# Kernel tuning notes

Hardware: AMD Instinct MI355X
Metric: run time of the kernel (lower is better)

## Reference

```python
import jax, jax.numpy as jnp
import numpy as np

B, C, H, W = 4, 12, 256, 256
ALPHA = 2.0
LARGE = 1e6  # > any image dimension; sentinel for 'no feature pixel found yet'


def _dist_1d(feature):
    # feature: [..., L] bool. 1D distance along last axis to nearest True element.
    f = jnp.moveaxis(feature, -1, 0)  # [L, ...]
    init = jnp.full(f.shape[1:], LARGE, jnp.float32)

    def step(c, fi):
        c = jnp.where(fi, 0.0, jnp.minimum(c + 1.0, LARGE))
        return c, c

    _, fwd = jax.lax.scan(step, init, f)
    _, bwd = jax.lax.scan(step, init, f[::-1])
    fwd = jnp.moveaxis(fwd, 0, -1)
    bwd = jnp.moveaxis(bwd[::-1], 0, -1)
    return jnp.minimum(fwd, bwd)


def edt(mask):
    # Exact Euclidean distance transform, matching scipy distance_transform_edt:
    # mask: [N, H, W] bool; returns distance from each pixel to nearest False pixel
    # (0 at False pixels). Separable squared-EDT: 1D pass along rows, then an
    # exact min over column offsets: D2[i,j] = min_j' g2[i,j'] + (j-j')**2.
    feature = ~mask
    g = _dist_1d(jnp.swapaxes(feature, -1, -2))  # distance along H within each column
    g = jnp.swapaxes(g, -1, -2)                  # [N, H, W]
    g2 = g * g
    Wd = mask.shape[-1]
    jidx = jnp.arange(Wd, dtype=jnp.float32)     # [W]
    cols = jnp.moveaxis(g2, -1, 0)               # [W, N, H]

    def step(running, xs):
        col, t = xs                              # col: [N, H], t: scalar
        cand = col[..., None] + (jidx - t) ** 2  # [N, H, W]
        return jnp.minimum(running, cand), None

    init = jnp.full(g2.shape, LARGE * LARGE, jnp.float32)
    d2, _ = jax.lax.scan(step, init, (cols, jidx))
    return jnp.sqrt(d2)


def distance_field(mask):
    # mask: [N, H, W] bool. field = edt(fg) + edt(bg); zero if no fg pixel (as in torch).
    field = edt(mask) + edt(~mask)
    has_fg = jnp.any(mask, axis=(-2, -1))
    return jnp.where(has_fg[..., None, None], field, 0.0)


def setup_inputs() -> dict:
    key = jax.random.key(0)
    k1, k2 = jax.random.split(key)
    pred = jax.random.normal(k1, (B, C, H, W), dtype=jnp.float32)
    target = jax.random.randint(k2, (B, H, W), 0, C, dtype=jnp.int64)
    return {"pred": pred, "target": target}


def reference(pred, target):
    pred_all = jax.nn.softmax(pred, axis=1)                              # [B,C,H,W]
    target_all = jax.nn.one_hot(target, C, dtype=pred.dtype, axis=1)     # [B,C,H,W]
    # Distance fields are computed under torch.no_grad() -> constants here.
    masks = jnp.stack([pred_all > 0.5, target_all > 0.5], 0).reshape(-1, H, W)
    fields = jax.lax.stop_gradient(distance_field(masks))
    fields = fields.reshape(2, pred.shape[0], C, H, W)
    pred_dt, target_dt = fields[0], fields[1]
    distance = pred_dt ** ALPHA + target_dt ** ALPHA
    pred_error = (pred_all - target_all) ** 2
    # per-class mean over (B,H,W), summed over classes (matches the torch loop)
    loss_sum = jnp.sum(jnp.mean(pred_error * distance, axis=(0, 2, 3)))
    logp = jax.nn.log_softmax(pred, axis=1)
    ce = -jnp.mean(jnp.take_along_axis(logp, target[:, None], axis=1))
    return loss_sum / C / pred.shape[0] / 3.0 + ce
```

## Files before the change

### kernel.cpp

```cpp
#include <hip/hip_runtime.h>
#include <math.h>

constexpr int Bn = 4, Cn = 12, Hn = 256, Wn = 256;
constexpr int HWn  = Hn * Wn;
constexpr int NPIX = Bn * HWn;
constexpr int NPLANE = Bn * Cn;
constexpr int NMASK = 2 * NPLANE;
constexpr int NJOB  = 2 * NMASK;
constexpr float LARGEf = 1.0e6f;


__global__ void masks_kernel(const float* __restrict__ pred,
                             const int* __restrict__ target,
                             unsigned int* __restrict__ maskw,
                             float* __restrict__ err,
                             unsigned int* __restrict__ blockOr,
                             double* __restrict__ cepart) {
    int pix = blockIdx.x * blockDim.x + threadIdx.x;
    int b = pix >> 16;
    int p = pix & (HWn - 1);
    float v[Cn];
    float mx = -3.4e38f;
#pragma unroll
    for (int c = 0; c < Cn; ++c) {
        v[c] = pred[(size_t)(b * Cn + c) * HWn + p];
        mx = fmaxf(mx, v[c]);
    }
    int t = target[pix];
    float raw_t = 0.f, s = 0.f;
#pragma unroll
    for (int c = 0; c < Cn; ++c) {
        if (c == t) raw_t = v[c];
        v[c] = expf(v[c] - mx);
        s += v[c];
    }
    unsigned word = 1u << (Cn + t);
#pragma unroll
    for (int c = 0; c < Cn; ++c) {
        float prob = v[c] / s;
        int pb = (prob > 0.5f) ? 1 : 0;
        word |= (unsigned)pb << c;
        float oh = (c == t) ? 1.0f : 0.0f;
        float d = prob - oh;
        err[(size_t)(b * Cn + c) * HWn + p] = d * d;
    }
    maskw[pix] = word;
    float logp_t = raw_t - mx - logf(s);

    unsigned worw = word;
    for (int o = 32; o > 0; o >>= 1) worw |= __shfl_down(worw, o, 64);
    double ced = (double)logp_t;
    for (int o = 32; o > 0; o >>= 1) ced += __shfl_down(ced, o, 64);
    int lane = threadIdx.x & 63, wv = threadIdx.x >> 6;
    if (lane == 0) {
        blockOr[blockIdx.x * 4 + wv] = worw;
        cepart[blockIdx.x * 4 + wv] = ced;
    }
}

__device__ __forceinline__ int mask_has_fg(const unsigned int* fgflags, int m) {
    int mm = (m < NPLANE) ? m : m - NPLANE;
    int b = mm / Cn, c = mm % Cn;
    unsigned fg = (m < NPLANE) ? fgflags[b] : fgflags[4 + b];
    return (fg >> c) & 1;
}

constexpr int SEG  = 4;
constexpr int SEGR = Hn / SEG;
constexpr int STRb = 68;

__global__ void colpass_kernel(const unsigned int* __restrict__ maskw,
                               const unsigned int* __restrict__ blockOr,
                               unsigned char* __restrict__ gcol,
                               unsigned int* __restrict__ colmask,
                               unsigned int* __restrict__ fgflags) {
    int blk = blockIdx.x;
    int tid = threadIdx.x;
    int lane = tid & 63, wv = tid >> 6;
    if (blk == NMASK * 4) {
        unsigned acc = 0;
#pragma unroll
        for (int k = 0; k < 16; ++k) acc |= blockOr[wv * 1024 + k * 64 + lane];
        for (int o = 32; o > 0; o >>= 1) acc |= __shfl_down(acc, o, 64);
        if (lane == 0) {
            fgflags[wv] = acc & 0xFFFu;
            fgflags[4 + wv] = acc >> Cn;
        }
        return;
    }
    int m  = blk >> 2;
    int cg = blk & 3;
    int mm = (m < NPLANE) ? m : m - NPLANE;
    int b = mm / Cn, c = mm % Cn;
    unsigned bit = (m < NPLANE) ? (unsigned)c : (unsigned)(Cn + c);
    int s  = wv;
    int jl = lane;
    int j  = cg * 64 + jl;
    int r0 = s * SEGR;
    const unsigned int* mp = maskw + (size_t)b * HWn;
    unsigned char* gpA = gcol + (size_t)m * HWn;
    unsigned char* gpB = gcol + (size_t)(m + NMASK) * HWn;

    __shared__ unsigned char ldsFA[256 * STRb];
    __shared__ unsigned char ldsFB[256 * STRb];
    __shared__ float eFA[256], eFB[256], eBA[256], eBB[256];
    __shared__ unsigned char segEmptyA[256], segEmptyB[256];

    unsigned long long vbits = 0ull;
    float cdA = LARGEf, cdB = LARGEf;
    for (int i = 0; i < SEGR; ++i) {
        unsigned w = mp[(r0 + i) * Wn + j];
        unsigned f = (w >> bit) & 1u;
        vbits |= (unsigned long long)f << i;
        cdA = (!f) ? 0.f : fminf(cdA + 1.f, LARGEf);
        cdB = f ? 0.f : fminf(cdB + 1.f, LARGEf);
        ldsFA[tid * STRb + i] = (unsigned char)fminf(cdA, 255.f);
        ldsFB[tid * STRb + i] = (unsigned char)fminf(cdB, 255.f);
    }
    unsigned long long aBits = ~vbits;
    eFA[tid] = cdA;
    eFB[tid] = cdB;
    eBA[tid] = aBits ? (float)__builtin_ctzll(aBits) : LARGEf;
    eBB[tid] = vbits ? (float)__builtin_ctzll(vbits) : LARGEf;
    segEmptyA[tid] = (aBits == 0ull) ? 1 : 0;
    segEmptyB[tid] = (vbits == 0ull) ? 1 : 0;
    __syncthreads();
    if (s == 0) {
        int emA = segEmptyA[jl] & segEmptyA[64 + jl] & segEmptyA[128 + jl] & segEmptyA[192 + jl];
        int emB = segEmptyB[jl] & segEmptyB[64 + jl] & segEmptyB[128 + jl] & segEmptyB[192 + jl];
        unsigned long long ba = __ballot(emA);
        unsigned long long bb = __ballot(emB);
        if (jl == 0) {
            colmask[m * 8 + cg * 2]                 = (unsigned)ba;
            colmask[m * 8 + cg * 2 + 1]             = (unsigned)(ba >> 32);
            colmask[(m + NMASK) * 8 + cg * 2]       = (unsigned)bb;
            colmask[(m + NMASK) * 8 + cg * 2 + 1]   = (unsigned)(bb >> 32);
        }
    }
    float xA = LARGEf, xB = LARGEf;
    for (int sp = 0; sp < s; ++sp) {
        xA = fminf(eFA[sp * 64 + jl], fminf(xA + (float)SEGR, LARGEf));
        xB = fminf(eFB[sp * 64 + jl], fminf(xB + (float)SEGR, LARGEf));
    }
    float yA = LARGEf, yB = LARGEf;
    for (int sp = SEG - 1; sp > s; --sp) {
        yA = fminf(eBA[sp * 64 + jl], fminf(yA + (float)SEGR, LARGEf));
        yB = fminf(eBB[sp * 64 + jl], fminf(yB + (float)SEGR, LARGEf));
    }
    float cA = LARGEf, cB = LARGEf;
    for (int i = SEGR - 1; i >= 0; --i) {
        unsigned f = (unsigned)((vbits >> i) & 1ull);
        cA = (!f) ? 0.f : fminf(cA + 1.f, LARGEf);
        cB = f ? 0.f : fminf(cB + 1.f, LARGEf);
        unsigned char ufA = ldsFA[tid * STRb + i];
        unsigned char ufB = ldsFB[tid * STRb + i];
        float lfA = (ufA == 255u) ? LARGEf : (float)ufA;
        float lfB = (ufB == 255u) ? LARGEf : (float)ufB;
        float fA = fminf(lfA, fminf(xA + (float)(i + 1), LARGEf));
        float wA = fminf(cA,  fminf(yA + (float)(SEGR - i), LARGEf));
        float gA = fminf(fA, wA);
        float fB = fminf(lfB, fminf(xB + (float)(i + 1), LARGEf));
        float wB = fminf(cB,  fminf(yB + (float)(SEGR - i), LARGEf));
        float gB = fminf(fB, wB);
        gpA[(r0 + i) * Wn + j] = (unsigned char)fminf(gA, 255.f);
        gpB[(r0 + i) * Wn + j] = (unsigned char)fminf(gB, 255.f);
    }
}

constexpr int RPAD = 256;
constexpr int NROWBLK = NMASK * Hn;
constexpr int RPB = 4;

__device__ __forceinline__ void scan4(const float* __restrict__ base, float m[4]) {
    float k2 = 1.f;
    for (int k = 1; k < Wn; k += 2) {
        float mx = fmaxf(fmaxf(m[0], m[1]), fmaxf(m[2], m[3]));
        if (k2 >= mx) break;
        float k2b = k2 + (float)(2 * k + 1);
#pragma unroll
        for (int g = 0; g < 4; ++g) {
            const float* p = base + 64 * g;
            m[g] = fminf(m[g], k2  + p[-k]);
            m[g] = fminf(m[g], k2b + p[-k - 1]);
            m[g] = fminf(m[g], k2  + p[k]);
            m[g] = fminf(m[g], k2b + p[k + 1]);
        }
        k2 = k2b + (float)(2 * k + 3);
    }
}

__global__ void rowpass_kernel(const unsigned char* __restrict__ gcol,
                               const unsigned int* __restrict__ colmask,
                               const float* __restrict__ err,
                               const unsigned int* __restrict__ fgflags,
                               double* __restrict__ partials) {
    int blk = blockIdx.x;
    int tid = threadIdx.x;
    int lane = tid & 63, w = tid >> 6;
    int m = (blk * RPB) >> 8;
    if (!mask_has_fg(fgflags, m)) {
        if (tid < RPB) partials[blk * RPB + tid] = 0.0;
        return;
    }
    int job = blk * RPB + w;
    int i = job & (Hn - 1);
    const float X = 1e12f;
    __shared__ float lds[RPB][2][Wn + 2 * RPAD];
    float* rA = lds[w][0];
    float* rB = lds[w][1];

    int ep = (m < NPLANE) ? m : m - NPLANE;
    const float* epr = err + (size_t)ep * HWn + i * Wn;
    float e0 = epr[lane], e1 = epr[lane + 64];
    float e2 = epr[lane + 128], e3 = epr[lane + 192];

    const unsigned char* rp = gcol + (size_t)m * HWn + i * Wn;
    const unsigned char* rq = gcol + (size_t)(m + NMASK) * HWn + i * Wn;
    unsigned ua4 = ((const unsigned*)rp)[lane];
    unsigned ub4 = ((const unsigned*)rq)[lane];
    unsigned nibA = (colmask[m * 8 + (lane >> 3)] >> ((lane & 7) * 4)) & 0xFu;
    unsigned nibB = (colmask[(m + NMASK) * 8 + (lane >> 3)] >> ((lane & 7) * 4)) & 0xFu;
    float4 fa, fb;
    {
        unsigned g0 = ua4 & 0xFFu, g1 = (ua4 >> 8) & 0xFFu;
        unsigned g2 = (ua4 >> 16) & 0xFFu, g3 = ua4 >> 24;
        fa.x = (nibA & 1u) ? X : (float)(g0 * g0);
        fa.y = (nibA & 2u) ? X : (float)(g1 * g1);
        fa.z = (nibA & 4u) ? X : (float)(g2 * g2);
        fa.w = (nibA & 8u) ? X : (float)(g3 * g3);
        g0 = ub4 & 0xFFu; g1 = (ub4 >> 8) & 0xFFu;
        g2 = (ub4 >> 16) & 0xFFu; g3 = ub4 >> 24;
        fb.x = (nibB & 1u) ? X : (float)(g0 * g0);
        fb.y = (nibB & 2u) ? X : (float)(g1 * g1);
        fb.z = (nibB & 4u) ? X : (float)(g2 * g2);
        fb.w = (nibB & 8u) ? X : (float)(g3 * g3);
    }
    float4 xv = make_float4(X, X, X, X);
    ((float4*)rA)[lane] = xv;
    ((float4*)(rA + RPAD))[lane] = fa;
    ((float4*)(rA + RPAD + Wn))[lane] = xv;
    ((float4*)rB)[lane] = xv;
    ((float4*)(rB + RPAD))[lane] = fb;
    ((float4*)(rB + RPAD + Wn))[lane] = xv;
    __syncthreads();

    float mA[4], mB[4];
#pragma unroll
    for (int g = 0; g < 4; ++g) {
        mA[g] = rA[RPAD + lane + 64 * g];
        mB[g] = rB[RPAD + lane + 64 * g];
    }
    scan4(rA + RPAD + lane, mA);
    scan4(rB + RPAD + lane, mB);

    float ev[4] = {e0, e1, e2, e3};
    double v = 0.0;
#pragma unroll
    for (int g = 0; g < 4; ++g) {
        float f = sqrtf(mA[g]) + sqrtf(mB[g]);
        v += (double)(ev[g] * (f * f));
    }
    for (int o = 32; o > 0; o >>= 1) v += __shfl_down(v, o, 64);
    if (lane == 0) partials[job] = v;
}

__global__ void final_kernel(const double* __restrict__ partials,
                             const double* __restrict__ cepart,
                             float* __restrict__ out) {
    int tid = threadIdx.x;
    double a = 0.0, ce = 0.0;
    for (int idx = tid; idx < NROWBLK; idx += 1024) a += partials[idx];
    for (int idx = tid; idx < 4096; idx += 1024) ce += cepart[idx];
    __shared__ double sa[1024], sc[1024];
    sa[tid] = a; sc[tid] = ce;
    __syncthreads();
    for (int s = 512; s > 0; s >>= 1) {
        if (tid < s) { sa[tid] += sa[tid + s]; sc[tid] += sc[tid + s]; }
        __syncthreads();
    }
    if (tid == 0) {
        double loss_sum = sa[0] / (double)NPIX;
        double cem = -sc[0] / (double)NPIX;
        double res = loss_sum / (double)Cn / (double)Bn / 3.0 + cem;
        out[0] = (float)res;
    }
}

extern "C" void kernel_launch(void* const* d_in, const int* in_sizes, int n_in,
                              void* d_out, int out_size, void* d_ws, size_t ws_size,
                              hipStream_t stream) {
    const float* pred  = (const float*)d_in[0];
    const int* target  = (const int*)d_in[1];
    float* out = (float*)d_out;
    char* ws = (char*)d_ws;

    unsigned int* maskw = (unsigned int*)ws;
    size_t off = (size_t)NPIX * 4;
    float* err = (float*)(ws + off);
    off += (size_t)NPLANE * HWn * 4;
    unsigned char* gcol = (unsigned char*)(ws + off);
    off += (size_t)NJOB * HWn;
    unsigned int* colmask = (unsigned int*)(ws + off);
    off += (size_t)NJOB * 8 * 4;
    unsigned int* fgflags = (unsigned int*)(ws + off);
    off += 512;
    unsigned int* blockOr = (unsigned int*)(ws + off);
    off += 4096 * 4;
    double* partials = (double*)(ws + off);
    off += (size_t)NROWBLK * 8;
    double* cepart = (double*)(ws + off);

    masks_kernel<<<NPIX / 256, 256, 0, stream>>>(pred, target, maskw, err,
                                                 blockOr, cepart);
    colpass_kernel<<<NMASK * 4 + 1, 256, 0, stream>>>(maskw, blockOr, gcol,
                                                      colmask, fgflags);
    rowpass_kernel<<<NROWBLK / RPB, 256, 0, stream>>>(gcol, colmask, err,
                                                      fgflags, partials);
    final_kernel<<<1, 1024, 0, stream>>>(partials, cepart, out);
}
```

Measured before the change: 65.43 us.

## Prune row distance scan using per-4-pixel block minima in LDS

Replaces the per-pixel outward offset scan with a scan over 4-pixel blocks. A shared per-block minimum array lets each lane skip loading a block whose minimum plus squared distance cannot beat the current best. It also drops the large padded row buffers in favour of a small padded block-min array, and uses float4 LDS reads. The data-dependent branches may cause wave divergence, which could offset the savings from skipped loads.

```diff
diff --git a/kernel.cpp b/kernel.cpp
--- a/kernel.cpp
+++ b/kernel.cpp
@@ -167,25 +167,58 @@
     }
 }
 
-constexpr int RPAD = 256;
 constexpr int NROWBLK = NMASK * Hn;
 constexpr int RPB = 4;
 
-__device__ __forceinline__ void scan4(const float* __restrict__ base, float m[4]) {
-    float k2 = 1.f;
-    for (int k = 1; k < Wn; k += 2) {
-        float mx = fmaxf(fmaxf(m[0], m[1]), fmaxf(m[2], m[3]));
-        if (k2 >= mx) break;
-        float k2b = k2 + (float)(2 * k + 1);
+__device__ __forceinline__ void scan_blocks(const float* __restrict__ row,
+                                            const float* __restrict__ bm,
+                                            int c, int q0, float m[4]) {
+    const float4* r4 = (const float4*)row;
+#pragma unroll
+    for (int g = 0; g < 4; ++g) {
+        float4 v = r4[q0 + 16 * g];
+        m[g] = v.x + (float)((c - 0) * (c - 0));
+        m[g] = fminf(m[g], v.y + (float)((c - 1) * (c - 1)));
+        m[g] = fminf(m[g], v.z + (float)((c - 2) * (c - 2)));
+        m[g] = fminf(m[g], v.w + (float)((c - 3) * (c - 3)));
+    }
+    for (int t = 1; t < 64; ++t) {
+        int dL = 4 * t - 3 + c;
+        int dR = 4 * t - c;
+        int dmn = dL < dR ? dL : dR;
+        float mmax = fmaxf(fmaxf(m[0], m[1]), fmaxf(m[2], m[3]));
+        if ((float)(dmn * dmn) >= mmax) break;
+        float dl2[4], dr2[4];
+#pragma unroll
+        for (int i = 0; i < 4; ++i) {
+            int dv = c + 4 * t - i;
+            dl2[i] = (float)(dv * dv);
+            int du = 4 * t + i - c;
+            dr2[i] = (float)(du * du);
+        }
+        float bL = bm[64 + q0 - t];
 #pragma unroll
         for (int g = 0; g < 4; ++g) {
-            const float* p = base + 64 * g;
-            m[g] = fminf(m[g], k2  + p[-k]);
-            m[g] = fminf(m[g], k2b + p[-k - 1]);
-            m[g] = fminf(m[g], k2  + p[k]);
-            m[g] = fminf(m[g], k2b + p[k + 1]);
+            int ql = q0 + 16 * g - t;
+            int qr = q0 + 16 * g + t;
+            float bl = bm[64 + ql];
+            float br = bm[64 + qr];
+            if (bl + dl2[3] < m[g]) {
+                float4 v = r4[ql];
+                m[g] = fminf(m[g], v.x + dl2[0]);
+                m[g] = fminf(m[g], v.y + dl2[1]);
+                m[g] = fminf(m[g], v.z + dl2[2]);
+                m[g] = fminf(m[g], v.w + dl2[3]);
+            }
+            if (br + dr2[0] < m[g]) {
+                float4 v = r4[qr];
+                m[g] = fminf(m[g], v.x + dr2[0]);
+                m[g] = fminf(m[g], v.y + dr2[1]);
+                m[g] = fminf(m[g], v.z + dr2[2]);
+                m[g] = fminf(m[g], v.w + dr2[3]);
+            }
         }
-        k2 = k2b + (float)(2 * k + 3);
+        (void)bL;
     }
 }
 
@@ -205,9 +238,12 @@
     int job = blk * RPB + w;
     int i = job & (Hn - 1);
     const float X = 1e12f;
-    __shared__ float lds[RPB][2][Wn + 2 * RPAD];
-    float* rA = lds[w][0];
-    float* rB = lds[w][1];
+    __shared__ __attribute__((aligned(16))) float ldsRow[RPB][2][Wn];
+    __shared__ float ldsBm[RPB][2][192];
+    float* rA = ldsRow[w][0];
+    float* rB = ldsRow[w][1];
+    float* bmA = ldsBm[w][0];
+    float* bmB = ldsBm[w][1];
 
     int ep = (m < NPLANE) ? m : m - NPLANE;
     const float* epr = err + (size_t)ep * HWn + i * Wn;
@@ -235,23 +271,19 @@
         fb.z = (nibB & 4u) ? X : (float)(g2 * g2);
         fb.w = (nibB & 8u) ? X : (float)(g3 * g3);
     }
-    float4 xv = make_float4(X, X, X, X);
-    ((float4*)rA)[lane] = xv;
-    ((float4*)(rA + RPAD))[lane] = fa;
-    ((float4*)(rA + RPAD + Wn))[lane] = xv;
-    ((float4*)rB)[lane] = xv;
-    ((float4*)(rB + RPAD))[lane] = fb;
-    ((float4*)(rB + RPAD + Wn))[lane] = xv;
+    ((float4*)rA)[lane] = fa;
+    ((float4*)rB)[lane] = fb;
+    bmA[64 + lane] = fminf(fminf(fa.x, fa.y), fminf(fa.z, fa.w));
+    bmB[64 + lane] = fminf(fminf(fb.x, fb.y), fminf(fb.z, fb.w));
+    bmA[lane] = X; bmA[128 + lane] = X;
+    bmB[lane] = X; bmB[128 + lane] = X;
     __syncthreads();
 
+    int c = lane & 3;
+    int q0 = lane >> 2;
     float mA[4], mB[4];
-#pragma unroll
-    for (int g = 0; g < 4; ++g) {
-        mA[g] = rA[RPAD + lane + 64 * g];
-        mB[g] = rB[RPAD + lane + 64 * g];
-    }
-    scan4(rA + RPAD + lane, mA);
-    scan4(rB + RPAD + lane, mB);
+    scan_blocks(rA, bmA, c, q0, mA);
+    scan_blocks(rB, bmB, c, q0, mB);
 
     float ev[4] = {e0, e1, e2, e3};
     double v = 0.0;
```

Result: slower. 67.28 us (+2.8%).
